# Kernel tuning notes

Measured on AMD Instinct MI355X. Metric: run time of the kernel, lower is better.

The kernel has to match this reference:

```python
import jax, jax.numpy as jnp
import numpy as np

B, C, H, W = 4, 48, 64, 64
HEADS, TOPK_ATTN = 8, 2
E, TOPK_MOE, DT = 16, 2, 512
LN_EPS = 1e-5


def conv2d(x, w, groups=1, pad=0):
    return jax.lax.conv_general_dilated(
        x, w, (1, 1), [(pad, pad), (pad, pad)],
        dimension_numbers=('NCHW', 'OIHW', 'NCHW'),
        feature_group_count=groups)


def layernorm_c(x, w, b):
    # LayerNorm over channel dim of NCHW (Restormer-style: b c h w -> b (hw) c)
    mu = x.mean(axis=1, keepdims=True)
    var = x.var(axis=1, keepdims=True)
    xn = (x - mu) * jax.lax.rsqrt(var + LN_EPS)
    return xn * w[None, :, None, None] + b[None, :, None, None]


def maxpool2(x):
    b, c, h, w = x.shape
    return x.reshape(b, c, h // 2, 2, w // 2, 2).max(axis=(3, 5))


def topk_gates(probs, k):
    # probs [..., n]; keep top-k probs, renormalize (MoH/MoE masked gating)
    n = probs.shape[-1]
    _, idx = jax.lax.top_k(probs, k)
    mask = jax.nn.one_hot(idx, n, dtype=probs.dtype).sum(axis=-2)
    mg = probs * mask
    return mg / jnp.maximum(mg.sum(axis=-1, keepdims=True), jnp.finfo(probs.dtype).eps)


def setup_inputs() -> dict:
    key = jax.random.key(0)
    ks = jax.random.split(key, 12)
    s = 0.05
    return {
        'x': jax.random.normal(ks[0], (B, C, H, W), jnp.float32),
        'text_feature': jax.random.normal(ks[1], (B, DT), jnp.float32),
        'task_id': 0,
        'ln1_w': jnp.ones((C,), jnp.float32), 'ln1_b': jnp.zeros((C,), jnp.float32),
        'ln2_w': jnp.ones((C,), jnp.float32), 'ln2_b': jnp.zeros((C,), jnp.float32),
        'qkv_w': jax.random.normal(ks[2], (3 * C, C, 1, 1), jnp.float32) * s,
        'qkv_dw_w': jax.random.normal(ks[3], (3 * C, 1, 3, 3), jnp.float32) * s,
        'proj_w': jax.random.normal(ks[4], (C, C, 1, 1), jnp.float32) * s,
        'router_w': jax.random.normal(ks[5], (HEADS, C, 1, 1), jnp.float32) * s,
        'gate_wx': jax.random.normal(ks[6], (C, E), jnp.float32) * s,
        'gate_wt': jax.random.normal(ks[7], (DT, E), jnp.float32) * s,
        'exp_w1': jax.random.normal(ks[8], (E, C, C, 3, 3), jnp.float32) * s,
        'exp_b1': jnp.zeros((E, C), jnp.float32),
        'exp_w2': jax.random.normal(ks[9], (E, C, C, 3, 3), jnp.float32) * s,
        'exp_b2': jnp.zeros((E, C), jnp.float32),
    }


def reference(x, text_feature, task_id, ln1_w, ln1_b, ln2_w, ln2_b,
              qkv_w, qkv_dw_w, proj_w, router_w, gate_wx, gate_wt,
              exp_w1, exp_b1, exp_w2, exp_b2):
    b, c, h, w = x.shape
    hd, n = c // HEADS, h * w

    # ---------- MoH MDTA attention ----------
    y = layernorm_c(x, ln1_w, ln1_b)
    qkv = conv2d(conv2d(y, qkv_w), qkv_dw_w, groups=3 * c, pad=1)
    q, k, v = jnp.split(qkv, 3, axis=1)
    q = q.reshape(b, HEADS, hd, n)
    k = k.reshape(b, HEADS, hd, n)
    v = v.reshape(b, HEADS, hd, n)
    q = q / jnp.maximum(jnp.linalg.norm(q, axis=-1, keepdims=True), 1e-12)
    k = k / jnp.maximum(jnp.linalg.norm(k, axis=-1, keepdims=True), 1e-12)
    attn = jnp.einsum('bhcn,bhdn->bhcd', q, k) * (hd ** -0.5)
    attn = jax.nn.softmax(attn, axis=-1)
    out = jnp.einsum('bhcd,bhdn->bhcn', attn, v)  # [b, heads, hd, n]

    # per-pixel head routing (task 0 router; eval mode -> no MI/aux loss)
    rl = conv2d(y, router_w).reshape(b, HEADS, n)
    probs_h = jax.nn.softmax(rl.transpose(0, 2, 1), axis=-1)  # [b, n, heads]
    g = topk_gates(probs_h, TOPK_ATTN).transpose(0, 2, 1)     # [b, heads, n]
    out = out * g[:, :, None, :]
    out = out.reshape(b, c, h, w)
    x = x + conv2d(out, proj_w)

    # ---------- heterogeneous MoE FFN ----------
    y = layernorm_c(x, ln2_w, ln2_b)
    pooled = y.mean(axis=(2, 3))                      # [b, c]
    logits = pooled @ gate_wx + text_feature @ gate_wt
    probs_e = jax.nn.softmax(logits, axis=-1)
    gates = topk_gates(probs_e, TOPK_MOE)             # [b, E], top-k sparse

    def block(z, w1, b1, w2, b2):
        hh = conv2d(z, w1, pad=1) + b1[None, :, None, None]
        hh = jax.nn.gelu(hh, approximate=False)
        return conv2d(hh, w2, pad=1) + b2[None, :, None, None]

    ffn = jnp.zeros_like(x)
    for e in range(E):
        t = e % 3
        if t == 0:  # NoRescaleExpert
            he = block(y, exp_w1[e], exp_b1[e], exp_w2[e], exp_b2[e])
        elif t == 1:  # UpThenDownExpert: nearest up x2 -> block -> maxpool
            z = jnp.repeat(jnp.repeat(y, 2, axis=2), 2, axis=3)
            he = maxpool2(block(z, exp_w1[e], exp_b1[e], exp_w2[e], exp_b2[e]))
        else:  # DownThenUpExpert: maxpool -> block -> bilinear up x2
            z = maxpool2(y)
            he = jax.image.resize(
                block(z, exp_w1[e], exp_b1[e], exp_w2[e], exp_b2[e]),
                x.shape, 'bilinear')
        # combine: zero-gated samples contribute exactly zero (== sparse dispatch)
        ffn = ffn + gates[:, e][:, None, None, None] * he

    return x + ffn
```

## Files before the change

kernel.cpp:

```cpp
#include <hip/hip_runtime.h>
#include <math.h>

#define SB 4
#define CC 48
#define NH 8
#define HDIM 6
#define NPIX 4096
#define NE 16
#define TD 512

__device__ __forceinline__ float wave_sum(float t){
#pragma unroll
  for (int o = 32; o >= 1; o >>= 1) t += __shfl_xor(t, o, 64);
  return t;
}

__device__ __forceinline__ float gelu(float t){
  return 0.5f*t*(1.f + erff(t*0.70710678118654752f));
}

#define ACC8(A, Z) { float _z=(Z); \
  A[0]+=_z*_w0.x; A[1]+=_z*_w0.y; A[2]+=_z*_w0.z; A[3]+=_z*_w0.w; \
  A[4]+=_z*_w1.x; A[5]+=_z*_w1.y; A[6]+=_z*_w1.z; A[7]+=_z*_w1.w; }

__global__ __launch_bounds__(256) void k_ln_qkv(
    const float* __restrict__ x, const float* __restrict__ ln1w, const float* __restrict__ ln1b,
    const float* __restrict__ qkvw, const float* __restrict__ routw,
    float* __restrict__ qkv_raw, float* __restrict__ rl)
{
  int sec = blockIdx.z;
  int NOC = (sec == 5) ? 32 : 24;
  __shared__ __align__(16) float wl[32*48];
  int tid = threadIdx.x;
  for (int i = tid; i < NOC*48; i += 256){
    int oc = i/48, c = i%48, og = sec*24 + oc;
    wl[i] = (og < 144) ? qkvw[og*48 + c] : routw[(og-144)*48 + c];
  }
  __syncthreads();
  int b = blockIdx.y;
  int p0 = blockIdx.x*512 + tid, p1 = p0 + 256;
  const float* xb = x + (size_t)b*CC*NPIX;
  float v0[48], v1[48];
  float mu0 = 0.f, mu1 = 0.f;
#pragma unroll
  for (int c = 0; c < CC; c++){
    v0[c] = xb[(size_t)c*NPIX + p0]; v1[c] = xb[(size_t)c*NPIX + p1];
    mu0 += v0[c]; mu1 += v1[c];
  }
  mu0 *= (1.f/CC); mu1 *= (1.f/CC);
  float va0 = 0.f, va1 = 0.f;
#pragma unroll
  for (int c = 0; c < CC; c++){
    float d0 = v0[c]-mu0, d1 = v1[c]-mu1; va0 += d0*d0; va1 += d1*d1;
  }
  float rs0 = rsqrtf(va0*(1.f/CC) + 1e-5f), rs1 = rsqrtf(va1*(1.f/CC) + 1e-5f);
#pragma unroll
  for (int c = 0; c < CC; c++){
    float w = ln1w[c], bb = ln1b[c];
    v0[c] = (v0[c]-mu0)*rs0*w + bb;
    v1[c] = (v1[c]-mu1)*rs1*w + bb;
  }
  float* qb = qkv_raw + (size_t)b*144*NPIX;
  float* rb = rl + (size_t)b*NH*NPIX;
  for (int oc = 0; oc < NOC; oc++){
    const float4* wv = (const float4*)&wl[oc*48];
    float s0 = 0.f, s1 = 0.f;
#pragma unroll
    for (int q = 0; q < 12; q++){
      float4 w = wv[q];
      s0 += w.x*v0[q*4] + w.y*v0[q*4+1] + w.z*v0[q*4+2] + w.w*v0[q*4+3];
      s1 += w.x*v1[q*4] + w.y*v1[q*4+1] + w.z*v1[q*4+2] + w.w*v1[q*4+3];
    }
    int og = sec*24 + oc;
    float* dst = (og < 144) ? (qb + (size_t)og*NPIX) : (rb + (size_t)(og-144)*NPIX);
    dst[p0] = s0; dst[p1] = s1;
  }
}

__global__ __launch_bounds__(256) void k_dwconv(
    const float* __restrict__ in, const float* __restrict__ w, float* __restrict__ out)
{
  int ch = blockIdx.y, b = blockIdx.z;
  int p = blockIdx.x*256 + threadIdx.x;
  int y = p >> 6, xx = p & 63;
  const float* wc = w + ch*9;
  const float* ib = in + ((size_t)b*144 + ch)*NPIX;
  float acc = 0.f;
#pragma unroll
  for (int ky = 0; ky < 3; ky++){
    int yy = y + ky - 1;
    if ((unsigned)yy < 64u){
#pragma unroll
      for (int kx = 0; kx < 3; kx++){
        int xc = xx + kx - 1;
        if ((unsigned)xc < 64u) acc += wc[ky*3+kx]*ib[yy*64+xc];
      }
    }
  }
  out[((size_t)b*144 + ch)*NPIX + p] = acc;
}

__global__ __launch_bounds__(256) void k_router_gates(
    const float* __restrict__ rl, float* __restrict__ g)
{
  int idx = blockIdx.x*256 + threadIdx.x;
  int b = idx >> 12, p = idx & (NPIX-1);
  const float* r = rl + (size_t)b*NH*NPIX + p;
  float l[NH];
  float mx = -1e30f;
#pragma unroll
  for (int h = 0; h < NH; h++){ l[h] = r[(size_t)h*NPIX]; mx = fmaxf(mx, l[h]); }
  float s = 0.f;
#pragma unroll
  for (int h = 0; h < NH; h++){ l[h] = __expf(l[h]-mx); s += l[h]; }
  int i1 = 0; float p1 = -1.f;
#pragma unroll
  for (int h = 0; h < NH; h++) if (l[h] > p1){ p1 = l[h]; i1 = h; }
  int i2 = -1; float p2 = -1.f;
#pragma unroll
  for (int h = 0; h < NH; h++) if (h != i1 && l[h] > p2){ p2 = l[h]; i2 = h; }
  float denom = p1 + p2;
  float* go = g + (size_t)b*NH*NPIX + p;
#pragma unroll
  for (int h = 0; h < NH; h++)
    go[(size_t)h*NPIX] = (h == i1 || h == i2) ? l[h]/denom : 0.f;
}

__global__ __launch_bounds__(256) void k_attn_part(
    const float* __restrict__ qkv, float* __restrict__ part)
{
  int ch = blockIdx.x, h = blockIdx.y, b = blockIdx.z;
  const float* q = qkv + ((size_t)b*144 + h*HDIM)*NPIX;
  const float* k = qkv + ((size_t)b*144 + 48 + h*HDIM)*NPIX;
  int tid = threadIdx.x;
  float qq[HDIM] = {0}, kk[HDIM] = {0}, qk[HDIM*HDIM] = {0};
#pragma unroll
  for (int t = 0; t < 2; t++){
    int n = ch*512 + t*256 + tid;
    float qv[HDIM], kv[HDIM];
#pragma unroll
    for (int c = 0; c < HDIM; c++){ qv[c] = q[(size_t)c*NPIX + n]; kv[c] = k[(size_t)c*NPIX + n]; }
#pragma unroll
    for (int c = 0; c < HDIM; c++){
      qq[c] += qv[c]*qv[c]; kk[c] += kv[c]*kv[c];
#pragma unroll
      for (int d = 0; d < HDIM; d++) qk[c*HDIM+d] += qv[c]*kv[d];
    }
  }
#pragma unroll
  for (int c = 0; c < HDIM; c++){ qq[c] = wave_sum(qq[c]); kk[c] = wave_sum(kk[c]); }
#pragma unroll
  for (int i = 0; i < HDIM*HDIM; i++) qk[i] = wave_sum(qk[i]);
  __shared__ float red[4][48];
  int lane = tid & 63, wv = tid >> 6;
  if (lane == 0){
#pragma unroll
    for (int c = 0; c < HDIM; c++){ red[wv][c] = qq[c]; red[wv][6+c] = kk[c]; }
#pragma unroll
    for (int i = 0; i < HDIM*HDIM; i++) red[wv][12+i] = qk[i];
  }
  __syncthreads();
  if (tid < 48)
    part[((size_t)(b*NH+h)*8 + ch)*48 + tid] = red[0][tid]+red[1][tid]+red[2][tid]+red[3][tid];
}

__global__ __launch_bounds__(64) void k_attn_soft(
    const float* __restrict__ part, float* __restrict__ smg)
{
  int h = blockIdx.x, b = blockIdx.y, tid = threadIdx.x;
  __shared__ float tot[48];
  if (tid < 48){
    float s = 0.f;
    for (int ch = 0; ch < 8; ch++) s += part[((size_t)(b*NH+h)*8 + ch)*48 + tid];
    tot[tid] = s;
  }
  __syncthreads();
  if (tid < HDIM){
    int c = tid;
    float qn = fmaxf(sqrtf(tot[c]), 1e-12f);
    float row[HDIM];
    float mx = -1e30f;
#pragma unroll
    for (int d = 0; d < HDIM; d++){
      float kn = fmaxf(sqrtf(tot[6+d]), 1e-12f);
      float a = tot[12 + c*HDIM + d] / (qn*kn) * 0.40824829046386307f;
      row[d] = a; mx = fmaxf(mx, a);
    }
    float s = 0.f;
#pragma unroll
    for (int d = 0; d < HDIM; d++){ row[d] = __expf(row[d]-mx); s += row[d]; }
#pragma unroll
    for (int d = 0; d < HDIM; d++) smg[(size_t)(b*NH+h)*36 + c*HDIM + d] = row[d]/s;
  }
}

__global__ __launch_bounds__(256) void k_attn_apply(
    const float* __restrict__ qkv, const float* __restrict__ smg,
    const float* __restrict__ g, float* __restrict__ out)
{
  int h = blockIdx.y, b = blockIdx.z;
  __shared__ float sm[36];
  int tid = threadIdx.x;
  if (tid < 36) sm[tid] = smg[(size_t)(b*NH+h)*36 + tid];
  __syncthreads();
  int n = blockIdx.x*256 + tid;
  const float* v = qkv + ((size_t)b*144 + 96 + h*HDIM)*NPIX;
  float vv[HDIM];
#pragma unroll
  for (int d = 0; d < HDIM; d++) vv[d] = v[(size_t)d*NPIX + n];
  float gg = g[((size_t)b*NH + h)*NPIX + n];
  float* ob = out + ((size_t)b*CC + h*HDIM)*NPIX;
#pragma unroll
  for (int c = 0; c < HDIM; c++){
    float o = 0.f;
#pragma unroll
    for (int d = 0; d < HDIM; d++) o += sm[c*HDIM+d]*vv[d];
    ob[(size_t)c*NPIX + n] = o*gg;
  }
}

__global__ __launch_bounds__(256) void k_proj_ln2(
    const float* __restrict__ attn_out, const float* __restrict__ x,
    const float* __restrict__ projw, const float* __restrict__ ln2w, const float* __restrict__ ln2b,
    float* __restrict__ xout, float* __restrict__ y2)
{
  __shared__ __align__(16) float w[CC*CC];
  int tid = threadIdx.x;
  for (int i = tid; i < CC*CC; i += 256) w[i] = projw[i];
  __syncthreads();
  int b = blockIdx.y;
  int p = blockIdx.x*256 + tid;
  const float* ain = attn_out + (size_t)b*CC*NPIX + p;
  float a[CC];
#pragma unroll
  for (int c = 0; c < CC; c++) a[c] = ain[(size_t)c*NPIX];
  const float* xb = x + (size_t)b*CC*NPIX + p;
  float xv[CC];
  float mu = 0.f;
#pragma unroll
  for (int oc = 0; oc < CC; oc++){
    const float4* wr = (const float4*)&w[oc*CC];
    float acc = 0.f;
#pragma unroll
    for (int q = 0; q < 12; q++){
      float4 ww = wr[q];
      acc += ww.x*a[q*4] + ww.y*a[q*4+1] + ww.z*a[q*4+2] + ww.w*a[q*4+3];
    }
    float t = xb[(size_t)oc*NPIX] + acc;
    xv[oc] = t; mu += t;
  }
  mu *= (1.f/CC);
  float var = 0.f;
#pragma unroll
  for (int c = 0; c < CC; c++){ float d = xv[c]-mu; var += d*d; }
  var *= (1.f/CC);
  float rs = rsqrtf(var + 1e-5f);
  float* xo = xout + (size_t)b*CC*NPIX + p;
  float* yo = y2 + (size_t)b*CC*NPIX + p;
#pragma unroll
  for (int c = 0; c < CC; c++){
    xo[(size_t)c*NPIX] = xv[c];
    yo[(size_t)c*NPIX] = (xv[c]-mu)*rs*ln2w[c] + ln2b[c];
  }
}

__global__ __launch_bounds__(256) void k_pool(const float* __restrict__ y2, float* __restrict__ pooled)
{
  int bc = blockIdx.x;
  const float* r = y2 + (size_t)bc*NPIX;
  float s = 0.f;
  for (int n = threadIdx.x; n < NPIX; n += 256) s += r[n];
  s = wave_sum(s);
  __shared__ float red[4];
  int lane = threadIdx.x & 63, wv = threadIdx.x >> 6;
  if (lane == 0) red[wv] = s;
  __syncthreads();
  if (threadIdx.x == 0) pooled[bc] = (red[0]+red[1]+red[2]+red[3]) * (1.f/NPIX);
}

__global__ __launch_bounds__(64) void k_moe_gate(
    const float* __restrict__ pooled, const float* __restrict__ text,
    const float* __restrict__ gwx, const float* __restrict__ gwt,
    float* __restrict__ gates, int* __restrict__ pairs)
{
  int tid = threadIdx.x;
  int b = tid >> 4, e = tid & 15;
  float acc = 0.f;
  for (int c = 0; c < CC; c++) acc += pooled[b*CC + c]*gwx[c*NE + e];
  for (int d = 0; d < TD; d++) acc += text[b*TD + d]*gwt[d*NE + e];
  __shared__ float lg[SB][NE];
  lg[b][e] = acc;
  __syncthreads();
  if (tid < SB){
    int bb = tid;
    float mx = -1e30f;
    for (int i = 0; i < NE; i++) mx = fmaxf(mx, lg[bb][i]);
    float ex[NE]; float s = 0.f;
    for (int i = 0; i < NE; i++){ ex[i] = __expf(lg[bb][i]-mx); s += ex[i]; }
    int i1 = 0; float p1 = -1.f;
    for (int i = 0; i < NE; i++) if (ex[i] > p1){ p1 = ex[i]; i1 = i; }
    int i2 = -1; float p2 = -1.f;
    for (int i = 0; i < NE; i++) if (i != i1 && ex[i] > p2){ p2 = ex[i]; i2 = i; }
    float denom = p1 + p2;
    for (int i = 0; i < NE; i++)
      gates[bb*NE + i] = (i == i1 || i == i2) ? ex[i]/denom : 0.f;
    pairs[bb*2 + 0] = bb*NE + i1;
    pairs[bb*2 + 1] = bb*NE + i2;
  }
}

__device__ __forceinline__ float* hslot(float* hb, int e, int b, int np){
  int t0c = (e+2)/3, t1c = (e+1)/3, t2c = e/3;
  size_t off = 4u*((size_t)t0c*196608u + (size_t)t1c*786432u + (size_t)t2c*49152u);
  return hb + off + (size_t)b*CC*np;
}

__global__ __launch_bounds__(256) void k_econv1u(
    const float* __restrict__ y2, const float* __restrict__ w1, const float* __restrict__ b1,
    const int* __restrict__ pairs, float* __restrict__ hbase)
{
  int pe = pairs[blockIdx.y];
  int b = pe >> 4, e = pe & 15, ty = e % 3;
  int nx = (ty == 0) ? 48 : ((ty == 1) ? 96 : 24);
  if ((int)blockIdx.x >= nx) return;
  int ocg = blockIdx.x % 6, band = blockIdx.x / 6, yb = band*8;
  int tid = threadIdx.x;

  __shared__ __align__(16) float smem[3456 + 2600];
  float* wl = smem; float* patch = smem + 3456;
  const float4* wv4 = (const float4*)wl;
  const float* wg = w1 + (size_t)e*CC*CC*9 + (size_t)(ocg*8)*CC*9;
  for (int i = tid; i < 3456; i += 256){
    int ic = i/72, r2 = i%72, k = r2/8, j = r2%8;
    wl[i] = wg[((size_t)j*CC + ic)*9 + k];
  }
  float bb[8];
#pragma unroll
  for (int j = 0; j < 8; j++) bb[j] = b1[e*CC + ocg*8 + j];
  const float* src = y2 + (size_t)b*CC*NPIX;

  if (ty == 0){
    float* hp = hslot(hbase, e, b, 4096);
    int r = tid >> 5, xp = (tid & 31)*2;
    float a0[8], a1[8];
#pragma unroll
    for (int j = 0; j < 8; j++){ a0[j] = bb[j]; a1[j] = bb[j]; }
    int ldso[10], srco[10];
#pragma unroll
    for (int q = 0; q < 10; q++){
      int i = tid + 256*q;
      int icl = i/640, rem = i%640, rr = rem>>6, cc = rem&63;
      int s = yb - 1 + rr;
      ldso[q] = icl*650 + rr*65 + cc;
      srco[q] = ((unsigned)s < 64u) ? (icl*NPIX + s*64 + cc) : -1;
    }
    float st[10];
#pragma unroll
    for (int q = 0; q < 10; q++) st[q] = (srco[q] >= 0) ? src[srco[q]] : 0.f;
    for (int icg = 0; icg < 12; icg++){
      __syncthreads();
#pragma unroll
      for (int q = 0; q < 10; q++) patch[ldso[q]] = st[q];
      if (icg < 11){
        const float* s2 = src + (size_t)(icg+1)*4*NPIX;
#pragma unroll
        for (int q = 0; q < 10; q++) st[q] = (srco[q] >= 0) ? s2[srco[q]] : 0.f;
      }
      __syncthreads();
#pragma unroll
      for (int icl = 0; icl < 4; icl++){
        const float* pp = patch + icl*650 + r*65;
        float zz[3][4];
#pragma unroll
        for (int dy = 0; dy < 3; dy++)
#pragma unroll
          for (int dx = 0; dx < 4; dx++){
            int xx = xp - 1 + dx;
            zz[dy][dx] = ((unsigned)xx < 64u) ? pp[dy*65 + xx] : 0.f;
          }
        int wb = ((icg*4+icl)*9)*2;
#pragma unroll
        for (int k = 0; k < 9; k++){
          float4 _w0 = wv4[wb + k*2], _w1 = wv4[wb + k*2 + 1];
          ACC8(a0, zz[k/3][k%3]);
          ACC8(a1, zz[k/3][k%3+1]);
        }
      }
    }
    int p0 = (yb + r)*64 + xp;
#pragma unroll
    for (int j = 0; j < 8; j++){
      int oc = ocg*8 + j;
      hp[(size_t)oc*4096 + p0]     = gelu(a0[j]);
      hp[(size_t)oc*4096 + p0 + 1] = gelu(a1[j]);
    }
  } else if (ty == 1){
    float* hp = hslot(hbase, e, b, 16384);
    int r = tid >> 5, xp = (tid & 31)*4;
    float ac[4][8];
#pragma unroll
    for (int i = 0; i < 4; i++)
#pragma unroll
      for (int j = 0; j < 8; j++) ac[i][j] = bb[j];
    int row0 = (yb >> 1) - 1;
    int ldso[6], srco[6];
#pragma unroll
    for (int q = 0; q < 6; q++){
      int i = tid + 256*q;
      int icl = i/384, rem = i%384, rr = rem>>6, cc = rem&63;
      int s = row0 + rr;
      ldso[q] = icl*390 + rr*65 + cc;
      srco[q] = ((unsigned)s < 64u) ? (icl*NPIX + s*64 + cc) : -1;
    }
    float st[6];
#pragma unroll
    for (int q = 0; q < 6; q++) st[q] = (srco[q] >= 0) ? src[srco[q]] : 0.f;
    for (int icg = 0; icg < 12; icg++){
      __syncthreads();
#pragma unroll
      for (int q = 0; q < 6; q++) patch[ldso[q]] = st[q];
      if (icg < 11){
        const float* s2 = src + (size_t)(icg+1)*4*NPIX;
#pragma unroll
        for (int q = 0; q < 6; q++) st[q] = (srco[q] >= 0) ? s2[srco[q]] : 0.f;
      }
      __syncthreads();
#pragma unroll
      for (int icl = 0; icl < 4; icl++){
        const float* pp = patch + icl*390;
        int lr[3];
#pragma unroll
        for (int dy = 0; dy < 3; dy++) lr[dy] = ((r + dy - 1) >> 1) + 1;
        float zz[3][6];
#pragma unroll
        for (int dy = 0; dy < 3; dy++)
#pragma unroll
          for (int dx = 0; dx < 6; dx++){
            int xx = xp - 1 + dx;
            zz[dy][dx] = ((unsigned)xx < 128u) ? pp[lr[dy]*65 + (xx>>1)] : 0.f;
          }
        int wb = ((icg*4+icl)*9)*2;
#pragma unroll
        for (int k = 0; k < 9; k++){
          float4 _w0 = wv4[wb + k*2], _w1 = wv4[wb + k*2 + 1];
          int ky = k/3, kx = k%3;
          ACC8(ac[0], zz[ky][kx]);
          ACC8(ac[1], zz[ky][kx+1]);
          ACC8(ac[2], zz[ky][kx+2]);
          ACC8(ac[3], zz[ky][kx+3]);
        }
      }
    }
#pragma unroll
    for (int i = 0; i < 4; i++){
      int p = (yb + r)*128 + xp + i;
#pragma unroll
      for (int j = 0; j < 8; j++)
        hp[(size_t)(ocg*8 + j)*16384 + p] = gelu(ac[i][j]);
    }
  } else {
    float* hp = hslot(hbase, e, b, 1024);
    int r = tid >> 5, xp = tid & 31;
    float ac[8];
#pragma unroll
    for (int j = 0; j < 8; j++) ac[j] = bb[j];
    int row0 = 2*yb - 2;
    int ldso[10], srco[10];
#pragma unroll
    for (int q = 0; q < 10; q++){
      int i = tid + 256*q;
      int icl = i/1280, rem = i%1280, rr = rem>>6, cc = rem&63;
      int s = row0 + rr;
      ldso[q] = icl*1300 + rr*65 + cc;
      srco[q] = ((unsigned)s < 64u) ? (icl*NPIX + s*64 + cc) : -1;
    }
    float st[10];
#pragma unroll
    for (int q = 0; q < 10; q++) st[q] = (srco[q] >= 0) ? src[srco[q]] : 0.f;
    for (int icg = 0; icg < 24; icg++){
      __syncthreads();
#pragma unroll
      for (int q = 0; q < 10; q++) patch[ldso[q]] = st[q];
      if (icg < 23){
        const float* s2 = src + (size_t)(icg+1)*2*NPIX;
#pragma unroll
        for (int q = 0; q < 10; q++) st[q] = (srco[q] >= 0) ? s2[srco[q]] : 0.f;
      }
      __syncthreads();
#pragma unroll
      for (int icl = 0; icl < 2; icl++){
        const float* pp = patch + icl*1300;
        float zz[3][3];
#pragma unroll
        for (int dy = 0; dy < 3; dy++){
          int sy = yb + r + dy - 1;
          int pr2 = 2*(r + dy - 1) + 2;
#pragma unroll
          for (int dx = 0; dx < 3; dx++){
            int sx = xp + dx - 1;
            float m = 0.f;
            if ((unsigned)sy < 32u && (unsigned)sx < 32u){
              int c2 = 2*sx;
              m = fmaxf(fmaxf(pp[pr2*65+c2], pp[pr2*65+c2+1]),
                        fmaxf(pp[(pr2+1)*65+c2], pp[(pr2+1)*65+c2+1]));
            }
            zz[dy][dx] = m;
          }
        }
        int wb = ((icg*2+icl)*9)*2;
#pragma unroll
        for (int k = 0; k < 9; k++){
          float4 _w0 = wv4[wb + k*2], _w1 = wv4[wb + k*2 + 1];
          ACC8(ac, zz[k/3][k%3]);
        }
      }
    }
    int p = (yb + r)*32 + xp;
#pragma unroll
    for (int j = 0; j < 8; j++)
      hp[(size_t)(ocg*8 + j)*1024 + p] = gelu(ac[j]);
  }
}

__device__ __forceinline__ void bl_coord(int o, int& i0, int& i1, float& w0, float& w1){
  float f = 0.5f*o - 0.25f;
  float fl = floorf(f);
  int i = (int)fl;
  float fr = f - fl;
  i0 = i < 0 ? 0 : i;
  int j = i + 1;
  i1 = j > 31 ? 31 : j;
  w0 = 1.f - fr; w1 = fr;
}

__global__ __launch_bounds__(256) void k_econv2u(
    const float* __restrict__ hbase, const float* __restrict__ w2, const float* __restrict__ b2,
    const float* __restrict__ gates, const int* __restrict__ pairs, float* __restrict__ out)
{
  int pe = pairs[blockIdx.y];
  int b = pe >> 4, e = pe & 15, ty = e % 3;
  int nx = (ty == 0) ? 48 : ((ty == 1) ? 96 : 6);
  if ((int)blockIdx.x >= nx) return;
  float gt = gates[b*NE + e];
  int ocg = (ty == 2) ? blockIdx.x : (blockIdx.x % 6);
  int band = (ty == 2) ? 0 : (blockIdx.x / 6);
  int yb = band*8;
  int tid = threadIdx.x;

  __shared__ __align__(16) float smem[3456 + 9216];
  float* wl = smem; float* patch = smem + 3456;
  const float4* wv4 = (const float4*)wl;
  const float* wg = w2 + (size_t)e*CC*CC*9 + (size_t)(ocg*8)*CC*9;
  for (int i = tid; i < 3456; i += 256){
    int ic = i/72, r2 = i%72, k = r2/8, j = r2%8;
    wl[i] = wg[((size_t)j*CC + ic)*9 + k];
  }
  float bb[8];
#pragma unroll
  for (int j = 0; j < 8; j++) bb[j] = b2[e*CC + ocg*8 + j];
  float* ob = out + (size_t)b*CC*NPIX;

  if (ty == 0){
    const float* src = hslot((float*)hbase, e, b, 4096);
    int r = tid >> 5, xp = (tid & 31)*2;
    float a0[8], a1[8];
#pragma unroll
    for (int j = 0; j < 8; j++){ a0[j] = bb[j]; a1[j] = bb[j]; }
    int ldso[10], srco[10];
#pragma unroll
    for (int q = 0; q < 10; q++){
      int i = tid + 256*q;
      int icl = i/640, rem = i%640, rr = rem>>6, cc = rem&63;
      int s = yb - 1 + rr;
      ldso[q] = icl*650 + rr*65 + cc;
      srco[q] = ((unsigned)s < 64u) ? (icl*4096 + s*64 + cc) : -1;
    }
    float st[10];
#pragma unroll
    for (int q = 0; q < 10; q++) st[q] = (srco[q] >= 0) ? src[srco[q]] : 0.f;
    for (int icg = 0; icg < 12; icg++){
      __syncthreads();
#pragma unroll
      for (int q = 0; q < 10; q++) patch[ldso[q]] = st[q];
      if (icg < 11){
        const float* s2 = src + (size_t)(icg+1)*4*4096;
#pragma unroll
        for (int q = 0; q < 10; q++) st[q] = (srco[q] >= 0) ? s2[srco[q]] : 0.f;
      }
      __syncthreads();
#pragma unroll
      for (int icl = 0; icl < 4; icl++){
        const float* pp = patch + icl*650 + r*65;
        float zz[3][4];
#pragma unroll
        for (int dy = 0; dy < 3; dy++)
#pragma unroll
          for (int dx = 0; dx < 4; dx++){
            int xx = xp - 1 + dx;
            zz[dy][dx] = ((unsigned)xx < 64u) ? pp[dy*65 + xx] : 0.f;
          }
        int wb = ((icg*4+icl)*9)*2;
#pragma unroll
        for (int k = 0; k < 9; k++){
          float4 _w0 = wv4[wb + k*2], _w1 = wv4[wb + k*2 + 1];
          ACC8(a0, zz[k/3][k%3]);
          ACC8(a1, zz[k/3][k%3+1]);
        }
      }
    }
    int p0 = (yb + r)*64 + xp;
#pragma unroll
    for (int j = 0; j < 8; j++){
      int oc = ocg*8 + j;
      atomicAdd(&ob[(size_t)oc*4096 + p0],     gt*a0[j]);
      atomicAdd(&ob[(size_t)oc*4096 + p0 + 1], gt*a1[j]);
    }
  } else if (ty == 1){
    const float* src = hslot((float*)hbase, e, b, 16384);
    int r = tid >> 5, xp = (tid & 31)*4;
    float ac[4][8];
#pragma unroll
    for (int i = 0; i < 4; i++)
#pragma unroll
      for (int j = 0; j < 8; j++) ac[i][j] = bb[j];
    int ldso[10], srco[10];
#pragma unroll
    for (int q = 0; q < 10; q++){
      int i = tid + 256*q;
      int icl = i/1280, rem = i%1280, rr = rem>>7, cc = rem&127;
      int s = yb - 1 + rr;
      ldso[q] = icl*1290 + rr*129 + cc;
      srco[q] = ((unsigned)s < 128u) ? (icl*16384 + s*128 + cc) : -1;
    }
    float st[10];
#pragma unroll
    for (int q = 0; q < 10; q++) st[q] = (srco[q] >= 0) ? src[srco[q]] : 0.f;
    for (int icg = 0; icg < 24; icg++){
      __syncthreads();
#pragma unroll
      for (int q = 0; q < 10; q++) patch[ldso[q]] = st[q];
      if (icg < 23){
        const float* s2 = src + (size_t)(icg+1)*2*16384;
#pragma unroll
        for (int q = 0; q < 10; q++) st[q] = (srco[q] >= 0) ? s2[srco[q]] : 0.f;
      }
      __syncthreads();
#pragma unroll
      for (int icl = 0; icl < 2; icl++){
        const float* pp = patch + icl*1290 + r*129;
        float zz[3][6];
#pragma unroll
        for (int dy = 0; dy < 3; dy++)
#pragma unroll
          for (int dx = 0; dx < 6; dx++){
            int xx = xp - 1 + dx;
            zz[dy][dx] = ((unsigned)xx < 128u) ? pp[dy*129 + xx] : 0.f;
          }
        int wb = ((icg*2+icl)*9)*2;
#pragma unroll
        for (int k = 0; k < 9; k++){
          float4 _w0 = wv4[wb + k*2], _w1 = wv4[wb + k*2 + 1];
          int ky = k/3, kx = k%3;
          ACC8(ac[0], zz[ky][kx]);
          ACC8(ac[1], zz[ky][kx+1]);
          ACC8(ac[2], zz[ky][kx+2]);
          ACC8(ac[3], zz[ky][kx+3]);
        }
      }
    }
    int pr = (yb + r) >> 1;
    int c0 = xp >> 1;
#pragma unroll
    for (int j = 0; j < 8; j++){
      float m0 = fmaxf(ac[0][j], ac[1][j]);
      float m1 = fmaxf(ac[2][j], ac[3][j]);
      float o0 = fmaxf(m0, __shfl_xor(m0, 32, 64));
      float o1 = fmaxf(m1, __shfl_xor(m1, 32, 64));
      if ((r & 1) == 0){
        int oc = ocg*8 + j;
        atomicAdd(&ob[(size_t)oc*4096 + pr*64 + c0],     gt*o0);
        atomicAdd(&ob[(size_t)oc*4096 + pr*64 + c0 + 1], gt*o1);
      }
    }
  } else {
    const float* src = hslot((float*)hbase, e, b, 1024);
    float ac[4][8];
#pragma unroll
    for (int i = 0; i < 4; i++)
#pragma unroll
      for (int j = 0; j < 8; j++) ac[i][j] = bb[j];
    float st[8];
#pragma unroll
    for (int q = 0; q < 8; q++){
      int i = tid + 256*q;
      st[q] = src[i];
    }
    for (int icg = 0; icg < 24; icg++){
      __syncthreads();
#pragma unroll
      for (int q = 0; q < 8; q++) patch[tid + 256*q] = st[q];
      if (icg < 23){
        const float* s2 = src + (size_t)(icg+1)*2*1024;
#pragma unroll
        for (int q = 0; q < 8; q++) st[q] = s2[tid + 256*q];
      }
      __syncthreads();
#pragma unroll
      for (int icl = 0; icl < 2; icl++){
        const float* pp = patch + icl*1024;
        int wb0 = ((icg*2+icl)*9)*2;
#pragma unroll
        for (int ii = 0; ii < 4; ii++){
          int l = tid + 256*ii;
          int oy = l >> 5, ox = l & 31;
#pragma unroll
          for (int k = 0; k < 9; k++){
            int ky = k/3, kx = k%3;
            int yy = oy + ky - 1, xx = ox + kx - 1;
            float z = ((unsigned)yy < 32u && (unsigned)xx < 32u) ? pp[yy*32 + xx] : 0.f;
            float4 _w0 = wv4[wb0 + k*2], _w1 = wv4[wb0 + k*2 + 1];
            ACC8(ac[ii], z);
          }
        }
      }
    }
    __syncthreads();
    float* he = patch;
#pragma unroll
    for (int ii = 0; ii < 4; ii++){
      int l = tid + 256*ii;
#pragma unroll
      for (int j = 0; j < 8; j++) he[l*9 + j] = ac[ii][j];
    }
    __syncthreads();
    for (int it = 0; it < 16; it++){
      int op = tid + 256*it;
      int y = op >> 6, x = op & 63;
      int y0,y1,x0,x1; float wy0,wy1,wx0,wx1;
      bl_coord(y, y0, y1, wy0, wy1);
      bl_coord(x, x0, x1, wx0, wx1);
#pragma unroll
      for (int j = 0; j < 8; j++){
        float v = wy0*(wx0*he[(y0*32+x0)*9+j] + wx1*he[(y0*32+x1)*9+j])
                + wy1*(wx0*he[(y1*32+x0)*9+j] + wx1*he[(y1*32+x1)*9+j]);
        int oc = ocg*8 + j;
        atomicAdd(&ob[(size_t)oc*NPIX + op], gt*v);
      }
    }
  }
}

extern "C" void kernel_launch(void* const* d_in, const int* in_sizes, int n_in,
                              void* d_out, int out_size, void* d_ws, size_t ws_size,
                              hipStream_t stream) {
  const float* x      = (const float*)d_in[0];
  const float* text   = (const float*)d_in[1];
  const float* ln1w   = (const float*)d_in[3];
  const float* ln1b   = (const float*)d_in[4];
  const float* ln2w   = (const float*)d_in[5];
  const float* ln2b   = (const float*)d_in[6];
  const float* qkvw   = (const float*)d_in[7];
  const float* qkvdw  = (const float*)d_in[8];
  const float* projw  = (const float*)d_in[9];
  const float* routw  = (const float*)d_in[10];
  const float* gwx    = (const float*)d_in[11];
  const float* gwt    = (const float*)d_in[12];
  const float* ew1    = (const float*)d_in[13];
  const float* eb1    = (const float*)d_in[14];
  const float* ew2    = (const float*)d_in[15];
  const float* eb2    = (const float*)d_in[16];
  float* out = (float*)d_out;

  float* wsf = (float*)d_ws;
  float* y2      = wsf;
  float* pooled  = wsf + 786432;
  float* gates   = wsf + 786624;
  int*   pairs   = (int*)(wsf + 786688);
  float* F       = wsf + 786944;
  float* qkv_raw = F;
  float* qkv_dw  = F + 2359296;
  float* rl      = F + 4718592;
  float* gmask   = F + 4849664;
  float* attnout = F + 4980736;
  float* part    = F + 5767168;
  float* smg     = F + 5779456;
  float* hbase   = F;

  k_ln_qkv<<<dim3(8, SB, 6), 256, 0, stream>>>(x, ln1w, ln1b, qkvw, routw, qkv_raw, rl);
  k_dwconv<<<dim3(16, 144, SB), 256, 0, stream>>>(qkv_raw, qkvdw, qkv_dw);
  k_router_gates<<<dim3(64), 256, 0, stream>>>(rl, gmask);
  k_attn_part<<<dim3(8, NH, SB), 256, 0, stream>>>(qkv_dw, part);
  k_attn_soft<<<dim3(NH, SB), 64, 0, stream>>>(part, smg);
  k_attn_apply<<<dim3(16, NH, SB), 256, 0, stream>>>(qkv_dw, smg, gmask, attnout);
  k_proj_ln2<<<dim3(16, SB), 256, 0, stream>>>(attnout, x, projw, ln2w, ln2b, out, y2);
  k_pool<<<dim3(SB*CC), 256, 0, stream>>>(y2, pooled);
  k_moe_gate<<<dim3(1), 64, 0, stream>>>(pooled, text, gwx, gwt, gates, pairs);

  k_econv1u<<<dim3(96, 8), 256, 0, stream>>>(y2, ew1, eb1, pairs, hbase);
  k_econv2u<<<dim3(96, 8), 256, 0, stream>>>(hbase, ew2, eb2, gates, pairs, out);

  (void)in_sizes; (void)n_in; (void)out_size; (void)ws_size;
}
```

Measured before the change: 387.6 us.

## Double-buffer expert conv patches, retile up-experts to 2x2, and widen grids

The expert conv kernels now keep two shared-memory patch buffers. The next input-channel group is stored while the current one is consumed, which removes one barrier per iteration. The upsample expert paths switch from 1x4 to 2x2 output micro-tiles, so the maxpool reduces inside the thread without a cross-lane shuffle and every thread does its own atomic. k_ln_qkv and k_proj_ln2 get smaller per-thread or per-block work so more blocks run, at the cost of more redundant weight loads into shared memory and a larger LDS footprint.

Measured after the change: 408.7 us. 1.05x slower.

```diff
diff --git a/kernel.cpp b/kernel.cpp
--- a/kernel.cpp
+++ b/kernel.cpp
@@ -38,42 +38,32 @@
   }
   __syncthreads();
   int b = blockIdx.y;
-  int p0 = blockIdx.x*512 + tid, p1 = p0 + 256;
+  int p = blockIdx.x*256 + tid;
   const float* xb = x + (size_t)b*CC*NPIX;
-  float v0[48], v1[48];
-  float mu0 = 0.f, mu1 = 0.f;
-#pragma unroll
-  for (int c = 0; c < CC; c++){
-    v0[c] = xb[(size_t)c*NPIX + p0]; v1[c] = xb[(size_t)c*NPIX + p1];
-    mu0 += v0[c]; mu1 += v1[c];
-  }
-  mu0 *= (1.f/CC); mu1 *= (1.f/CC);
-  float va0 = 0.f, va1 = 0.f;
-#pragma unroll
-  for (int c = 0; c < CC; c++){
-    float d0 = v0[c]-mu0, d1 = v1[c]-mu1; va0 += d0*d0; va1 += d1*d1;
-  }
-  float rs0 = rsqrtf(va0*(1.f/CC) + 1e-5f), rs1 = rsqrtf(va1*(1.f/CC) + 1e-5f);
-#pragma unroll
-  for (int c = 0; c < CC; c++){
-    float w = ln1w[c], bb = ln1b[c];
-    v0[c] = (v0[c]-mu0)*rs0*w + bb;
-    v1[c] = (v1[c]-mu1)*rs1*w + bb;
-  }
+  float v[48];
+  float mu = 0.f;
+#pragma unroll
+  for (int c = 0; c < CC; c++){ v[c] = xb[(size_t)c*NPIX + p]; mu += v[c]; }
+  mu *= (1.f/CC);
+  float va = 0.f;
+#pragma unroll
+  for (int c = 0; c < CC; c++){ float d = v[c]-mu; va += d*d; }
+  float rs = rsqrtf(va*(1.f/CC) + 1e-5f);
+#pragma unroll
+  for (int c = 0; c < CC; c++) v[c] = (v[c]-mu)*rs*ln1w[c] + ln1b[c];
   float* qb = qkv_raw + (size_t)b*144*NPIX;
   float* rb = rl + (size_t)b*NH*NPIX;
   for (int oc = 0; oc < NOC; oc++){
     const float4* wv = (const float4*)&wl[oc*48];
-    float s0 = 0.f, s1 = 0.f;
+    float s = 0.f;
 #pragma unroll
     for (int q = 0; q < 12; q++){
       float4 w = wv[q];
-      s0 += w.x*v0[q*4] + w.y*v0[q*4+1] + w.z*v0[q*4+2] + w.w*v0[q*4+3];
-      s1 += w.x*v1[q*4] + w.y*v1[q*4+1] + w.z*v1[q*4+2] + w.w*v1[q*4+3];
+      s += w.x*v[q*4] + w.y*v[q*4+1] + w.z*v[q*4+2] + w.w*v[q*4+3];
     }
     int og = sec*24 + oc;
     float* dst = (og < 144) ? (qb + (size_t)og*NPIX) : (rb + (size_t)(og-144)*NPIX);
-    dst[p0] = s0; dst[p1] = s1;
+    dst[p] = s;
   }
 }
 
@@ -219,17 +209,17 @@
   }
 }
 
-__global__ __launch_bounds__(256) void k_proj_ln2(
+__global__ __launch_bounds__(64) void k_proj_ln2(
     const float* __restrict__ attn_out, const float* __restrict__ x,
     const float* __restrict__ projw, const float* __restrict__ ln2w, const float* __restrict__ ln2b,
     float* __restrict__ xout, float* __restrict__ y2)
 {
   __shared__ __align__(16) float w[CC*CC];
   int tid = threadIdx.x;
-  for (int i = tid; i < CC*CC; i += 256) w[i] = projw[i];
+  for (int i = tid; i < CC*CC; i += 64) w[i] = projw[i];
   __syncthreads();
   int b = blockIdx.y;
-  int p = blockIdx.x*256 + tid;
+  int p = blockIdx.x*64 + tid;
   const float* ain = attn_out + (size_t)b*CC*NPIX + p;
   float a[CC];
 #pragma unroll
@@ -326,8 +316,8 @@
   int ocg = blockIdx.x % 6, band = blockIdx.x / 6, yb = band*8;
   int tid = threadIdx.x;
 
-  __shared__ __align__(16) float smem[3456 + 2600];
-  float* wl = smem; float* patch = smem + 3456;
+  __shared__ __align__(16) float smem[3456 + 5200];
+  float* wl = smem; float* pa = smem + 3456;
   const float4* wv4 = (const float4*)wl;
   const float* wg = w1 + (size_t)e*CC*CC*9 + (size_t)(ocg*8)*CC*9;
   for (int i = tid; i < 3456; i += 256){
@@ -357,19 +347,19 @@
     float st[10];
 #pragma unroll
     for (int q = 0; q < 10; q++) st[q] = (srco[q] >= 0) ? src[srco[q]] : 0.f;
+#pragma unroll
+    for (int q = 0; q < 10; q++) pa[ldso[q]] = st[q];
+    __syncthreads();
     for (int icg = 0; icg < 12; icg++){
-      __syncthreads();
-#pragma unroll
-      for (int q = 0; q < 10; q++) patch[ldso[q]] = st[q];
       if (icg < 11){
         const float* s2 = src + (size_t)(icg+1)*4*NPIX;
 #pragma unroll
         for (int q = 0; q < 10; q++) st[q] = (srco[q] >= 0) ? s2[srco[q]] : 0.f;
       }
-      __syncthreads();
+      const float* pcur = pa + (icg & 1)*2600;
 #pragma unroll
       for (int icl = 0; icl < 4; icl++){
-        const float* pp = patch + icl*650 + r*65;
+        const float* pp = pcur + icl*650 + r*65;
         float zz[3][4];
 #pragma unroll
         for (int dy = 0; dy < 3; dy++)
@@ -386,6 +376,12 @@
           ACC8(a1, zz[k/3][k%3+1]);
         }
       }
+      if (icg < 11){
+        float* pnext = pa + ((icg+1) & 1)*2600;
+#pragma unroll
+        for (int q = 0; q < 10; q++) pnext[ldso[q]] = st[q];
+      }
+      __syncthreads();
     }
     int p0 = (yb + r)*64 + xp;
 #pragma unroll
@@ -396,7 +392,7 @@
     }
   } else if (ty == 1){
     float* hp = hslot(hbase, e, b, 16384);
-    int r = tid >> 5, xp = (tid & 31)*4;
+    int qr = tid >> 6, qx = (tid & 63)*2;
     float ac[4][8];
 #pragma unroll
     for (int i = 0; i < 4; i++)
@@ -415,29 +411,29 @@
     float st[6];
 #pragma unroll
     for (int q = 0; q < 6; q++) st[q] = (srco[q] >= 0) ? src[srco[q]] : 0.f;
+#pragma unroll
+    for (int q = 0; q < 6; q++) pa[ldso[q]] = st[q];
+    __syncthreads();
+    int prw[4];
+#pragma unroll
+    for (int dy = 0; dy < 4; dy++) prw[dy] = ((2*qr + dy - 1) >> 1) + 1;
     for (int icg = 0; icg < 12; icg++){
-      __syncthreads();
-#pragma unroll
-      for (int q = 0; q < 6; q++) patch[ldso[q]] = st[q];
       if (icg < 11){
         const float* s2 = src + (size_t)(icg+1)*4*NPIX;
 #pragma unroll
         for (int q = 0; q < 6; q++) st[q] = (srco[q] >= 0) ? s2[srco[q]] : 0.f;
       }
-      __syncthreads();
+      const float* pcur = pa + (icg & 1)*1560;
 #pragma unroll
       for (int icl = 0; icl < 4; icl++){
-        const float* pp = patch + icl*390;
-        int lr[3];
-#pragma unroll
-        for (int dy = 0; dy < 3; dy++) lr[dy] = ((r + dy - 1) >> 1) + 1;
-        float zz[3][6];
-#pragma unroll
-        for (int dy = 0; dy < 3; dy++)
-#pragma unroll
-          for (int dx = 0; dx < 6; dx++){
-            int xx = xp - 1 + dx;
-            zz[dy][dx] = ((unsigned)xx < 128u) ? pp[lr[dy]*65 + (xx>>1)] : 0.f;
+        const float* pp = pcur + icl*390;
+        float zz[4][4];
+#pragma unroll
+        for (int dy = 0; dy < 4; dy++)
+#pragma unroll
+          for (int dx = 0; dx < 4; dx++){
+            int xx = qx + dx - 1;
+            zz[dy][dx] = ((unsigned)xx < 128u) ? pp[prw[dy]*65 + (xx>>1)] : 0.f;
           }
         int wb = ((icg*4+icl)*9)*2;
 #pragma unroll
@@ -446,14 +442,20 @@
           int ky = k/3, kx = k%3;
           ACC8(ac[0], zz[ky][kx]);
           ACC8(ac[1], zz[ky][kx+1]);
-          ACC8(ac[2], zz[ky][kx+2]);
-          ACC8(ac[3], zz[ky][kx+3]);
+          ACC8(ac[2], zz[ky+1][kx]);
+          ACC8(ac[3], zz[ky+1][kx+1]);
         }
       }
+      if (icg < 11){
+        float* pnext = pa + ((icg+1) & 1)*1560;
+#pragma unroll
+        for (int q = 0; q < 6; q++) pnext[ldso[q]] = st[q];
+      }
+      __syncthreads();
     }
 #pragma unroll
     for (int i = 0; i < 4; i++){
-      int p = (yb + r)*128 + xp + i;
+      int p = (yb + 2*qr + (i>>1))*128 + qx + (i&1);
 #pragma unroll
       for (int j = 0; j < 8; j++)
         hp[(size_t)(ocg*8 + j)*16384 + p] = gelu(ac[i][j]);
@@ -477,19 +479,19 @@
     float st[10];
 #pragma unroll
     for (int q = 0; q < 10; q++) st[q] = (srco[q] >= 0) ? src[srco[q]] : 0.f;
+#pragma unroll
+    for (int q = 0; q < 10; q++) pa[ldso[q]] = st[q];
+    __syncthreads();
     for (int icg = 0; icg < 24; icg++){
-      __syncthreads();
-#pragma unroll
-      for (int q = 0; q < 10; q++) patch[ldso[q]] = st[q];
       if (icg < 23){
         const float* s2 = src + (size_t)(icg+1)*2*NPIX;
 #pragma unroll
         for (int q = 0; q < 10; q++) st[q] = (srco[q] >= 0) ? s2[srco[q]] : 0.f;
       }
-      __syncthreads();
+      const float* pcur = pa + (icg & 1)*2600;
 #pragma unroll
       for (int icl = 0; icl < 2; icl++){
-        const float* pp = patch + icl*1300;
+        const float* pp = pcur + icl*1300;
         float zz[3][3];
 #pragma unroll
         for (int dy = 0; dy < 3; dy++){
@@ -514,6 +516,12 @@
           ACC8(ac, zz[k/3][k%3]);
         }
       }
+      if (icg < 23){
+        float* pnext = pa + ((icg+1) & 1)*2600;
+#pragma unroll
+        for (int q = 0; q < 10; q++) pnext[ldso[q]] = st[q];
+      }
+      __syncthreads();
     }
     int p = (yb + r)*32 + xp;
 #pragma unroll
@@ -548,7 +556,7 @@
   int tid = threadIdx.x;
 
   __shared__ __align__(16) float smem[3456 + 9216];
-  float* wl = smem; float* patch = smem + 3456;
+  float* wl = smem; float* pa = smem + 3456;
   const float4* wv4 = (const float4*)wl;
   const float* wg = w2 + (size_t)e*CC*CC*9 + (size_t)(ocg*8)*CC*9;
   for (int i = tid; i < 3456; i += 256){
@@ -578,19 +586,19 @@
     float st[10];
 #pragma unroll
     for (int q = 0; q < 10; q++) st[q] = (srco[q] >= 0) ? src[srco[q]] : 0.f;
+#pragma unroll
+    for (int q = 0; q < 10; q++) pa[ldso[q]] = st[q];
+    __syncthreads();
     for (int icg = 0; icg < 12; icg++){
-      __syncthreads();
-#pragma unroll
-      for (int q = 0; q < 10; q++) patch[ldso[q]] = st[q];
       if (icg < 11){
         const float* s2 = src + (size_t)(icg+1)*4*4096;
 #pragma unroll
         for (int q = 0; q < 10; q++) st[q] = (srco[q] >= 0) ? s2[srco[q]] : 0.f;
       }
-      __syncthreads();
+      const float* pcur = pa + (icg & 1)*2600;
 #pragma unroll
       for (int icl = 0; icl < 4; icl++){
-        const float* pp = patch + icl*650 + r*65;
+        const float* pp = pcur + icl*650 + r*65;
         float zz[3][4];
 #pragma unroll
         for (int dy = 0; dy < 3; dy++)
@@ -607,6 +615,12 @@
           ACC8(a1, zz[k/3][k%3+1]);
         }
       }
+      if (icg < 11){
+        float* pnext = pa + ((icg+1) & 1)*2600;
+#pragma unroll
+        for (int q = 0; q < 10; q++) pnext[ldso[q]] = st[q];
+      }
+      __syncthreads();
     }
     int p0 = (yb + r)*64 + xp;
 #pragma unroll
@@ -617,7 +631,7 @@
     }
   } else if (ty == 1){
     const float* src = hslot((float*)hbase, e, b, 16384);
-    int r = tid >> 5, xp = (tid & 31)*4;
+    int qr = tid >> 6, qx = (tid & 63)*2;
     float ac[4][8];
 #pragma unroll
     for (int i = 0; i < 4; i++)
@@ -635,26 +649,26 @@
     float st[10];
 #pragma unroll
     for (int q = 0; q < 10; q++) st[q] = (srco[q] >= 0) ? src[srco[q]] : 0.f;
+#pragma unroll
+    for (int q = 0; q < 10; q++) pa[ldso[q]] = st[q];
+    __syncthreads();
     for (int icg = 0; icg < 24; icg++){
-      __syncthreads();
-#pragma unroll
-      for (int q = 0; q < 10; q++) patch[ldso[q]] = st[q];
       if (icg < 23){
         const float* s2 = src + (size_t)(icg+1)*2*16384;
 #pragma unroll
         for (int q = 0; q < 10; q++) st[q] = (srco[q] >= 0) ? s2[srco[q]] : 0.f;
       }
-      __syncthreads();
+      const float* pcur = pa + (icg & 1)*2580;
 #pragma unroll
       for (int icl = 0; icl < 2; icl++){
-        const float* pp = patch + icl*1290 + r*129;
-        float zz[3][6];
-#pragma unroll
-        for (int dy = 0; dy < 3; dy++)
-#pragma unroll
-          for (int dx = 0; dx < 6; dx++){
-            int xx = xp - 1 + dx;
-            zz[dy][dx] = ((unsigned)xx < 128u) ? pp[dy*129 + xx] : 0.f;
+        const float* pp = pcur + icl*1290;
+        float zz[4][4];
+#pragma unroll
+        for (int dy = 0; dy < 4; dy++)
+#pragma unroll
+          for (int dx = 0; dx < 4; dx++){
+            int xx = qx + dx - 1;
+            zz[dy][dx] = ((unsigned)xx < 128u) ? pp[(2*qr + dy)*129 + xx] : 0.f;
           }
         int wb = ((icg*2+icl)*9)*2;
 #pragma unroll
@@ -663,24 +677,22 @@
           int ky = k/3, kx = k%3;
           ACC8(ac[0], zz[ky][kx]);
           ACC8(ac[1], zz[ky][kx+1]);
-          ACC8(ac[2], zz[ky][kx+2]);
-          ACC8(ac[3], zz[ky][kx+3]);
+          ACC8(ac[2], zz[ky+1][kx]);
+          ACC8(ac[3], zz[ky+1][kx+1]);
         }
       }
-    }
-    int pr = (yb + r) >> 1;
-    int c0 = xp >> 1;
+      if (icg < 23){
+        float* pnext = pa + ((icg+1) & 1)*2580;
+#pragma unroll
+        for (int q = 0; q < 10; q++) pnext[ldso[q]] = st[q];
+      }
+      __syncthreads();
+    }
+    int pr = (yb >> 1) + qr, pc = tid & 63;
 #pragma unroll
     for (int j = 0; j < 8; j++){
-      float m0 = fmaxf(ac[0][j], ac[1][j]);
-      float m1 = fmaxf(ac[2][j], ac[3][j]);
-      float o0 = fmaxf(m0, __shfl_xor(m0, 32, 64));
-      float o1 = fmaxf(m1, __shfl_xor(m1, 32, 64));
-      if ((r & 1) == 0){
-        int oc = ocg*8 + j;
-        atomicAdd(&ob[(size_t)oc*4096 + pr*64 + c0],     gt*o0);
-        atomicAdd(&ob[(size_t)oc*4096 + pr*64 + c0 + 1], gt*o1);
-      }
+      float m = fmaxf(fmaxf(ac[0][j], ac[1][j]), fmaxf(ac[2][j], ac[3][j]));
+      atomicAdd(&ob[(size_t)(ocg*8 + j)*4096 + pr*64 + pc], gt*m);
     }
   } else {
     const float* src = hslot((float*)hbase, e, b, 1024);
@@ -691,23 +703,20 @@
       for (int j = 0; j < 8; j++) ac[i][j] = bb[j];
     float st[8];
 #pragma unroll
-    for (int q = 0; q < 8; q++){
-      int i = tid + 256*q;
-      st[q] = src[i];
-    }
+    for (int q = 0; q < 8; q++) st[q] = src[tid + 256*q];
+#pragma unroll
+    for (int q = 0; q < 8; q++) pa[tid + 256*q] = st[q];
+    __syncthreads();
     for (int icg = 0; icg < 24; icg++){
-      __syncthreads();
-#pragma unroll
-      for (int q = 0; q < 8; q++) patch[tid + 256*q] = st[q];
       if (icg < 23){
         const float* s2 = src + (size_t)(icg+1)*2*1024;
 #pragma unroll
         for (int q = 0; q < 8; q++) st[q] = s2[tid + 256*q];
       }
-      __syncthreads();
+      const float* pcur = pa + (icg & 1)*2048;
 #pragma unroll
       for (int icl = 0; icl < 2; icl++){
-        const float* pp = patch + icl*1024;
+        const float* pp = pcur + icl*1024;
         int wb0 = ((icg*2+icl)*9)*2;
 #pragma unroll
         for (int ii = 0; ii < 4; ii++){
@@ -723,9 +732,14 @@
           }
         }
       }
-    }
-    __syncthreads();
-    float* he = patch;
+      if (icg < 23){
+        float* pnext = pa + ((icg+1) & 1)*2048;
+#pragma unroll
+        for (int q = 0; q < 8; q++) pnext[tid + 256*q] = st[q];
+      }
+      __syncthreads();
+    }
+    float* he = pa;
 #pragma unroll
     for (int ii = 0; ii < 4; ii++){
       int l = tid + 256*ii;
@@ -743,8 +757,7 @@
       for (int j = 0; j < 8; j++){
         float v = wy0*(wx0*he[(y0*32+x0)*9+j] + wx1*he[(y0*32+x1)*9+j])
                 + wy1*(wx0*he[(y1*32+x0)*9+j] + wx1*he[(y1*32+x1)*9+j]);
-        int oc = ocg*8 + j;
-        atomicAdd(&ob[(size_t)oc*NPIX + op], gt*v);
+        atomicAdd(&ob[(size_t)(ocg*8 + j)*NPIX + op], gt*v);
       }
     }
   }
@@ -786,13 +799,13 @@
   float* smg     = F + 5779456;
   float* hbase   = F;
 
-  k_ln_qkv<<<dim3(8, SB, 6), 256, 0, stream>>>(x, ln1w, ln1b, qkvw, routw, qkv_raw, rl);
+  k_ln_qkv<<<dim3(16, SB, 6), 256, 0, stream>>>(x, ln1w, ln1b, qkvw, routw, qkv_raw, rl);
   k_dwconv<<<dim3(16, 144, SB), 256, 0, stream>>>(qkv_raw, qkvdw, qkv_dw);
   k_router_gates<<<dim3(64), 256, 0, stream>>>(rl, gmask);
   k_attn_part<<<dim3(8, NH, SB), 256, 0, stream>>>(qkv_dw, part);
   k_attn_soft<<<dim3(NH, SB), 64, 0, stream>>>(part, smg);
   k_attn_apply<<<dim3(16, NH, SB), 256, 0, stream>>>(qkv_dw, smg, gmask, attnout);
-  k_proj_ln2<<<dim3(16, SB), 256, 0, stream>>>(attnout, x, projw, ln2w, ln2b, out, y2);
+  k_proj_ln2<<<dim3(64, SB), 64, 0, stream>>>(attnout, x, projw, ln2w, ln2b, out, y2);
   k_pool<<<dim3(SB*CC), 256, 0, stream>>>(y2, pooled);
   k_moe_gate<<<dim3(1), 64, 0, stream>>>(pooled, text, gwx, gwt, gates, pairs);
 
```
